# Performance work log

Hardware: AMD Instinct MI355X
Metric: run time of the kernel (lower is better)

## Reference

```python
import jax, jax.numpy as jnp
import numpy as np

N, D, E, R, G, M = 8192, 1024, 64, 64, 8, 8

def setup_inputs() -> dict:
    key = jax.random.key(0)
    k_h, k_wg, k_wl, k_w1, k_w2 = jax.random.split(key, 5)
    return {
        'h': jax.random.normal(k_h, (N, D), jnp.float32),
        'Wg': jax.random.normal(k_wg, (D, G), jnp.float32) * 0.02,  # nn.Linear weight (transposed)
        'bg': jnp.zeros((G,), jnp.float32),
        'Wloc': jax.random.normal(k_wl, (G, D, M), jnp.float32) * 0.02,
        'W1': jax.random.normal(k_w1, (E, D, R), jnp.float32) * 0.02,
        'W2': jax.random.normal(k_w2, (E, R, D), jnp.float32) * 0.02,
        'k': 2,
    }

def reference(h, Wg, bg, Wloc, W1, W2, k):
    n, d = h.shape
    g, _, m = Wloc.shape
    e = W1.shape[0]
    router_temp = 1.0
    # stage 1: group routing (top-1)
    g_scores = h @ Wg + bg                                   # (N, G)
    group_idx = jnp.argmax(g_scores, axis=-1)                # (N,)
    # stage 2: within-group scores; compute all groups (cheap: N*G*M) then select
    all_local = jnp.einsum('nd,gdm->ngm', h, Wloc)           # (N, G, M)
    local_scores = jnp.take_along_axis(all_local, group_idx[:, None, None], axis=1)[:, 0]  # (N, M)
    topv, topm = jax.lax.top_k(local_scores, k)              # (N, k)
    gate = jax.nn.softmax(topv / max(router_temp, 1e-6), axis=-1)
    expert_ids = group_idx[:, None] * m + topm               # (N, k) global expert ids
    # scatter gates into dense (N, E); topm entries are distinct per token
    gate_full = jnp.zeros((n, e), h.dtype).at[jnp.arange(n)[:, None], expert_ids].set(gate)
    # low-rank expert compute: relu(h @ W1) @ W2, weighted-combined
    tmp = jax.nn.relu(jnp.einsum('nd,edr->ner', h, W1))      # (N, E, R)
    out = jnp.einsum('ner,erd->nd', gate_full[:, :, None] * tmp, W2)  # (N, D)
    return out, expert_ids, gate, group_idx
```

## Files before the change

kernel.cpp:

```cpp
#include <hip/hip_runtime.h>
#include <hip/hip_bf16.h>
#include <cstdint>
#include <cstddef>

#define NTOK 8192
#define DIM  1024
#define NEXP 64
#define RANK 64
#define NGRP 8
#define NLOC 8

typedef __attribute__((ext_vector_type(8))) short bf16x8;
typedef __attribute__((ext_vector_type(4))) float f32x4;

static __device__ inline unsigned int pack_bf16x2(float a, float b) {
    __hip_bfloat16 ha = __float2bfloat16(a);
    __hip_bfloat16 hb = __float2bfloat16(b);
    return (unsigned int)(*(unsigned short*)&ha) |
           ((unsigned int)(*(unsigned short*)&hb) << 16);
}

__global__ __launch_bounds__(256, 4) void score_fused(
    const float* __restrict__ h, const float* __restrict__ Wg,
    const float* __restrict__ bg, const float* __restrict__ Wloc,
    unsigned short* __restrict__ hb, float* __restrict__ out_gidx,
    float* __restrict__ out_eid, float* __restrict__ out_gate,
    int* __restrict__ ws_eids, float* __restrict__ ws_gates,
    int* __restrict__ counts_e)
{
    __shared__ float Hs[16][66];
    __shared__ float Bs[64 * 8];
    __shared__ float Sp[16][16][8];
    __shared__ float Sg[16][9];
    __shared__ int   gsel[16];

    const int t0  = blockIdx.x * 16;
    const int tid = threadIdx.x;
    const int t   = tid & 15;
    const int kq  = tid >> 4;
    const int kbase = (kq >> 2) * 16 + (kq & 3);

    float acc[8] = {};
    for (int kc = 0; kc < DIM; kc += 64) {
        __syncthreads();
        {
            const int r = tid >> 4, c4 = tid & 15;
            const float4 v = *(const float4*)(h + (size_t)(t0 + r) * DIM + kc + c4 * 4);
            *(float2*)&Hs[r][c4 * 4]     = make_float2(v.x, v.y);
            *(float2*)&Hs[r][c4 * 4 + 2] = make_float2(v.z, v.w);
            uint2 pk;
            pk.x = pack_bf16x2(v.x, v.y);
            pk.y = pack_bf16x2(v.z, v.w);
            *(uint2*)(hb + (size_t)(t0 + r) * DIM + kc + c4 * 4) = pk;
        }
        {
            const float* src = Wg + (size_t)kc * NGRP;
            Bs[tid] = src[tid];
            Bs[tid + 256] = src[tid + 256];
        }
        __syncthreads();
#pragma unroll
        for (int kk = 0; kk < 4; ++kk) {
            const int k = kbase + kk * 4;
            const float a = Hs[t][k];
            const float4 b0 = *(const float4*)&Bs[k * 8];
            const float4 b1 = *(const float4*)&Bs[k * 8 + 4];
            acc[0] += a * b0.x; acc[1] += a * b0.y; acc[2] += a * b0.z; acc[3] += a * b0.w;
            acc[4] += a * b1.x; acc[5] += a * b1.y; acc[6] += a * b1.z; acc[7] += a * b1.w;
        }
    }
#pragma unroll
    for (int m = 0; m < 8; ++m) Sp[t][kq][m] = acc[m];
    __syncthreads();
    if (tid < 128) {
        const int tt = tid >> 3, m = tid & 7;
        float s = 0.f;
#pragma unroll
        for (int q = 0; q < 16; ++q) s += Sp[tt][q][m];
        Sg[tt][m] = s + bg[m];
    }
    __syncthreads();
    if (tid < 16) {
        int gi = 0; float best = Sg[tid][0];
#pragma unroll
        for (int g = 1; g < NGRP; ++g) {
            if (Sg[tid][g] > best) { best = Sg[tid][g]; gi = g; }
        }
        out_gidx[t0 + tid] = (float)gi;
        gsel[tid] = gi;
    }
    __syncthreads();

    {
        const int gsel_t = gsel[t];
        const float* wl = Wloc + (size_t)gsel_t * DIM * NLOC;
        const float* hrow = h + (size_t)(t0 + t) * DIM;
        float acc2[8] = {};
        for (int kc = DIM - 64; kc >= 0; kc -= 64) {
            const int k0 = kc + kq * 4;
            const f32x4 hv = *(const f32x4*)(hrow + k0);
#pragma unroll
            for (int kk = 0; kk < 4; ++kk) {
                const float a = hv[kk];
                const float4 b0 = *(const float4*)(wl + (size_t)(k0 + kk) * NLOC);
                const float4 b1 = *(const float4*)(wl + (size_t)(k0 + kk) * NLOC + 4);
                acc2[0] += a * b0.x; acc2[1] += a * b0.y; acc2[2] += a * b0.z; acc2[3] += a * b0.w;
                acc2[4] += a * b1.x; acc2[5] += a * b1.y; acc2[6] += a * b1.z; acc2[7] += a * b1.w;
            }
        }
#pragma unroll
        for (int m = 0; m < 8; ++m) Sp[t][kq][m] = acc2[m];
    }
    __syncthreads();
    if (tid < 128) {
        const int tt = tid >> 3, m = tid & 7;
        float s = 0.f;
#pragma unroll
        for (int q = 0; q < 16; ++q) s += Sp[tt][q][m];
        Sg[tt][m] = s;
    }
    __syncthreads();

    if (tid < 16) {
        const int tok = t0 + tid;
        float ls[NLOC];
#pragma unroll
        for (int m = 0; m < NLOC; ++m) ls[m] = Sg[tid][m];

        int m1 = 0; float v1 = ls[0];
#pragma unroll
        for (int m = 1; m < NLOC; ++m) { if (ls[m] > v1) { v1 = ls[m]; m1 = m; } }
        int m2 = (m1 == 0) ? 1 : 0; float v2 = ls[m2];
#pragma unroll
        for (int m = 0; m < NLOC; ++m) {
            if (m != m1 && m != ((m1 == 0) ? 1 : 0) && ls[m] > v2) { v2 = ls[m]; m2 = m; }
        }
        const float e2v = expf(v2 - v1);
        const float inv = 1.f / (1.f + e2v);
        const float g0 = inv, g1 = e2v * inv;
        const int gi = gsel[tid];
        const int ea = gi * NLOC + m1, eb = gi * NLOC + m2;

        out_eid[tok * 2 + 0] = (float)ea;
        out_eid[tok * 2 + 1] = (float)eb;
        out_gate[tok * 2 + 0] = g0;
        out_gate[tok * 2 + 1] = g1;
        ws_eids[tok * 2 + 0] = ea;
        ws_eids[tok * 2 + 1] = eb;
        ws_gates[tok * 2 + 0] = g0;
        ws_gates[tok * 2 + 1] = g1;
        atomicAdd(&counts_e[ea], 1);
        atomicAdd(&counts_e[eb], 1);
    }
}

__global__ __launch_bounds__(256) void scatter_e(
    const int* __restrict__ ws_eids, const float* __restrict__ ws_gates,
    const int* __restrict__ counts_e, int* __restrict__ cursor,
    int* __restrict__ token_list, float* __restrict__ slot_gate)
{
    __shared__ int offS[64];
    const int tid = threadIdx.x;
    if (tid < 64) {
        const int c = counts_e[tid];
        int s = c;
#pragma unroll
        for (int d = 1; d < 64; d <<= 1) {
            int v = __shfl_up(s, d, 64);
            if (tid >= d) s += v;
        }
        offS[tid] = s - c;
    }
    __syncthreads();
    const int t = blockIdx.x * 256 + tid;
    if (t >= NTOK) return;
#pragma unroll
    for (int j = 0; j < 2; ++j) {
        const int eid = ws_eids[t * 2 + j];
        const int pos = offS[eid] + atomicAdd(&cursor[eid], 1);
        token_list[pos] = t * 2 + j;
        slot_gate[pos] = ws_gates[t * 2 + j];
    }
}

__global__ __launch_bounds__(256) void prep_w(
    const float* __restrict__ W1, const float* __restrict__ W2,
    unsigned short* __restrict__ W1t, unsigned short* __restrict__ W2t)
{
    __shared__ float Ls[64][65];
    const int e = blockIdx.x;
    const int y = blockIdx.y;
    if (y < 16) {
        const int kb = y;
        const float* src = W1 + (size_t)e * DIM * RANK + (size_t)kb * 64 * RANK;
#pragma unroll
        for (int it = 0; it < 4; ++it) {
            const int kk = (threadIdx.x >> 4) + it * 16;
            const int rr = (threadIdx.x & 15) * 4;
            *(float4*)&Ls[kk][rr] = *(const float4*)(src + (size_t)kk * RANK + rr);
        }
        __syncthreads();
#pragma unroll
        for (int it = 0; it < 2; ++it) {
            const int idx = threadIdx.x + it * 256;
            const int r = idx >> 3, k8 = (idx & 7) * 8;
            uint4 v;
            v.x = pack_bf16x2(Ls[k8 + 0][r], Ls[k8 + 1][r]);
            v.y = pack_bf16x2(Ls[k8 + 2][r], Ls[k8 + 3][r]);
            v.z = pack_bf16x2(Ls[k8 + 4][r], Ls[k8 + 5][r]);
            v.w = pack_bf16x2(Ls[k8 + 6][r], Ls[k8 + 7][r]);
            *(uint4*)(W1t + (size_t)e * RANK * DIM + (size_t)r * DIM + kb * 64 + k8) = v;
        }
    } else {
        const int db = y - 16;
        const float* src = W2 + (size_t)e * RANK * DIM + db * 64;
#pragma unroll
        for (int it = 0; it < 4; ++it) {
            const int rr = (threadIdx.x >> 4) + it * 16;
            const int dd = (threadIdx.x & 15) * 4;
            *(float4*)&Ls[rr][dd] = *(const float4*)(src + (size_t)rr * DIM + dd);
        }
        __syncthreads();
#pragma unroll
        for (int it = 0; it < 2; ++it) {
            const int idx = threadIdx.x + it * 256;
            const int d = idx >> 3, r8 = (idx & 7) * 8;
            uint4 v;
            v.x = pack_bf16x2(Ls[r8 + 0][d], Ls[r8 + 1][d]);
            v.y = pack_bf16x2(Ls[r8 + 2][d], Ls[r8 + 3][d]);
            v.z = pack_bf16x2(Ls[r8 + 4][d], Ls[r8 + 5][d]);
            v.w = pack_bf16x2(Ls[r8 + 6][d], Ls[r8 + 7][d]);
            *(uint4*)(W2t + (size_t)e * DIM * RANK + (size_t)(db * 64 + d) * RANK + r8) = v;
        }
    }
}

__global__ __launch_bounds__(256, 2) void e1_mfma(
    const unsigned short* __restrict__ hb, const unsigned short* __restrict__ W1t,
    const int* __restrict__ counts_e, const int* __restrict__ token_list,
    const float* __restrict__ slot_gate, unsigned short* __restrict__ P)
{
    __shared__ unsigned short Hs[64 * 72];
    __shared__ unsigned short Ws[64 * 72];
    __shared__ int   tokS[64];
    __shared__ float gateS[64];
    __shared__ int   offS[65];

    const int e   = blockIdx.x;
    const int tid = threadIdx.x;
    if (tid < 64) {
        const int c = counts_e[tid];
        int s = c;
#pragma unroll
        for (int d = 1; d < 64; d <<= 1) {
            int v = __shfl_up(s, d, 64);
            if (tid >= d) s += v;
        }
        offS[tid] = s - c;
        if (tid == 63) offS[64] = s;
    }
    __syncthreads();
    const int n0 = offS[e];
    const int ne = offS[e + 1] - n0;

    const unsigned short* W1te = W1t + (size_t)e * RANK * DIM;
    const int wave = tid >> 6;
    const int lane = tid & 63;
    const int tx   = lane & 15;
    const int quad = lane >> 4;

    for (int tile = blockIdx.y; tile * 64 < ne; tile += 8) {
        const int row0 = tile * 64;
        __syncthreads();
        if (tid < 64) {
            const int gr = row0 + tid;
            tokS[tid]  = (gr < ne) ? token_list[n0 + gr] : -1;
            gateS[tid] = (gr < ne) ? slot_gate[n0 + gr] : 0.f;
        }
        f32x4 acc[4] = {};
        for (int kc = 0; kc < DIM; kc += 64) {
            __syncthreads();
#pragma unroll
            for (int it = 0; it < 2; ++it) {
                const int idx = tid + it * 256;
                const int s = idx >> 3, k8 = (idx & 7) * 8;
                const int ent = tokS[s];
                uint4 v = make_uint4(0, 0, 0, 0);
                if (ent >= 0)
                    v = *(const uint4*)(hb + (size_t)(ent >> 1) * DIM + kc + k8);
                *(uint4*)(Hs + s * 72 + k8) = v;
            }
#pragma unroll
            for (int it = 0; it < 2; ++it) {
                const int idx = tid + it * 256;
                const int r = idx >> 3, k8 = (idx & 7) * 8;
                *(uint4*)(Ws + r * 72 + k8) =
                    *(const uint4*)(W1te + (size_t)r * DIM + kc + k8);
            }
            __syncthreads();
#pragma unroll
            for (int ks = 0; ks < 2; ++ks) {
                const bf16x8 a = *(const bf16x8*)(Hs + (wave * 16 + tx) * 72 + ks * 32 + quad * 8);
#pragma unroll
                for (int j = 0; j < 4; ++j) {
                    const bf16x8 b = *(const bf16x8*)(Ws + (j * 16 + tx) * 72 + ks * 32 + quad * 8);
                    acc[j] = __builtin_amdgcn_mfma_f32_16x16x32_bf16(a, b, acc[j], 0, 0, 0);
                }
            }
        }
#pragma unroll
        for (int j = 0; j < 4; ++j) {
#pragma unroll
            for (int i = 0; i < 4; ++i) {
                const int sl = wave * 16 + quad * 4 + i;
                const int gr = row0 + sl;
                if (gr < ne) {
                    const float v = fmaxf(acc[j][i], 0.f) * gateS[sl];
                    __hip_bfloat16 hv = __float2bfloat16(v);
                    P[(size_t)(n0 + gr) * RANK + j * 16 + tx] = *(unsigned short*)&hv;
                }
            }
        }
    }
}

__global__ __launch_bounds__(256, 2) void e2_mfma(
    const unsigned short* __restrict__ P, const unsigned short* __restrict__ W2t,
    const int* __restrict__ counts_e, const int* __restrict__ token_list,
    float* __restrict__ out, float* __restrict__ contrib)
{
    __shared__ unsigned short Ps[64 * 72];
    __shared__ unsigned short W2s[64 * 72];
    __shared__ int tokS[64];
    __shared__ int offS[65];

    const int e = blockIdx.x;
    const int colbase = blockIdx.y * 64;
    const int tid = threadIdx.x;
    if (tid < 64) {
        const int c = counts_e[tid];
        int s = c;
#pragma unroll
        for (int d = 1; d < 64; d <<= 1) {
            int v = __shfl_up(s, d, 64);
            if (tid >= d) s += v;
        }
        offS[tid] = s - c;
        if (tid == 63) offS[64] = s;
    }
    __syncthreads();
    const int n0 = offS[e];
    const int ne = offS[e + 1] - n0;

    const unsigned short* W2te = W2t + (size_t)e * DIM * RANK;
    const int wave = tid >> 6;
    const int lane = tid & 63;
    const int tx   = lane & 15;
    const int quad = lane >> 4;

#pragma unroll
    for (int it = 0; it < 2; ++it) {
        const int idx = tid + it * 256;
        const int d = idx >> 3, r8 = (idx & 7) * 8;
        *(uint4*)(W2s + d * 72 + r8) =
            *(const uint4*)(W2te + (size_t)(colbase + d) * RANK + r8);
    }

    for (int tile = blockIdx.z; tile * 64 < ne; tile += 4) {
        const int row0 = tile * 64;
        __syncthreads();
        if (tid < 64) {
            const int gr = row0 + tid;
            tokS[tid] = (gr < ne) ? token_list[n0 + gr] : -1;
        }
#pragma unroll
        for (int it = 0; it < 2; ++it) {
            const int idx = tid + it * 256;
            const int s = idx >> 3, r8 = (idx & 7) * 8;
            const int gr = row0 + s;
            uint4 v = make_uint4(0, 0, 0, 0);
            if (gr < ne) v = *(const uint4*)(P + (size_t)(n0 + gr) * RANK + r8);
            *(uint4*)(Ps + s * 72 + r8) = v;
        }
        __syncthreads();
        f32x4 acc[4] = {};
#pragma unroll
        for (int ks = 0; ks < 2; ++ks) {
            const bf16x8 a = *(const bf16x8*)(Ps + (wave * 16 + tx) * 72 + ks * 32 + quad * 8);
#pragma unroll
            for (int j = 0; j < 4; ++j) {
                const bf16x8 b = *(const bf16x8*)(W2s + (j * 16 + tx) * 72 + ks * 32 + quad * 8);
                acc[j] = __builtin_amdgcn_mfma_f32_16x16x32_bf16(a, b, acc[j], 0, 0, 0);
            }
        }
#pragma unroll
        for (int i = 0; i < 4; ++i) {
            const int sl = wave * 16 + quad * 4 + i;
            const int ent = tokS[sl];
            if (ent >= 0) {
                float* base = (ent & 1) ? contrib : out;
                float* op = base + (size_t)(ent >> 1) * DIM + colbase;
#pragma unroll
                for (int j = 0; j < 4; ++j)
                    op[j * 16 + tx] = acc[j][i];
            }
        }
    }
}

__global__ __launch_bounds__(256) void combine_kernel(
    const float* __restrict__ contrib, float* __restrict__ out)
{
    const size_t i = (size_t)blockIdx.x * 256 + threadIdx.x;
    float4 a = ((const float4*)out)[i];
    const float4 b = ((const float4*)contrib)[i];
    a.x += b.x; a.y += b.y; a.z += b.z; a.w += b.w;
    ((float4*)out)[i] = a;
}

extern "C" void kernel_launch(void* const* d_in, const int* in_sizes, int n_in,
                              void* d_out, int out_size, void* d_ws, size_t ws_size,
                              hipStream_t stream)
{
    const float* h    = (const float*)d_in[0];
    const float* Wg   = (const float*)d_in[1];
    const float* bg   = (const float*)d_in[2];
    const float* Wloc = (const float*)d_in[3];
    const float* W1   = (const float*)d_in[4];
    const float* W2   = (const float*)d_in[5];

    float* out_f    = (float*)d_out;
    float* out_main = out_f;
    float* out_eid  = out_f + (size_t)NTOK * DIM;
    float* out_gate = out_eid + (size_t)NTOK * 2;
    float* out_gidx = out_gate + (size_t)NTOK * 2;

    int* ws_i        = (int*)d_ws;
    int* counts_e    = ws_i;
    int* cursor_e    = ws_i + 192;
    int* ws_eids     = ws_i + 16896;
    int* token_list  = ws_i + 33280;
    float* ws_f      = (float*)(ws_i + 49664);
    float* ws_gates  = ws_f;
    float* slot_gate = ws_f + 16384;
    unsigned short* P_h = (unsigned short*)(ws_f + 2 * 16384 + 65536);
    unsigned short* W1t = P_h + (size_t)16384 * RANK;
    unsigned short* W2t = W1t + (size_t)NEXP * RANK * DIM;
    float* contrib      = (float*)(W2t + (size_t)NEXP * DIM * RANK);
    unsigned short* hb = (unsigned short*)contrib;

    hipMemsetAsync(ws_i, 0, 256 * sizeof(int), stream);

    prep_w<<<dim3(NEXP, 32), 256, 0, stream>>>(W1, W2, W1t, W2t);
    score_fused<<<NTOK / 16, 256, 0, stream>>>(h, Wg, bg, Wloc, hb,
        out_gidx, out_eid, out_gate, ws_eids, ws_gates, counts_e);
    scatter_e<<<NTOK / 256, 256, 0, stream>>>(ws_eids, ws_gates, counts_e,
        cursor_e, token_list, slot_gate);
    e1_mfma<<<dim3(NEXP, 8), 256, 0, stream>>>(hb, W1t, counts_e, token_list,
        slot_gate, P_h);
    e2_mfma<<<dim3(NEXP, 16, 4), 256, 0, stream>>>(P_h, W2t, counts_e, token_list,
        out_main, contrib);
    combine_kernel<<<(NTOK * DIM / 4) / 256, 256, 0, stream>>>(contrib, out_main);
}
```

Baseline: 263.7 us.

## Restructure routing kernel to one wavefront per token with shuffle reductions

```diff
diff --git a/kernel.cpp b/kernel.cpp
--- a/kernel.cpp
+++ b/kernel.cpp
@@ -20,7 +20,7 @@
            ((unsigned int)(*(unsigned short*)&hb) << 16);
 }
 
-__global__ __launch_bounds__(256, 4) void score_fused(
+__global__ __launch_bounds__(256, 8) void score_route(
     const float* __restrict__ h, const float* __restrict__ Wg,
     const float* __restrict__ bg, const float* __restrict__ Wloc,
     unsigned short* __restrict__ hb, float* __restrict__ out_gidx,
@@ -28,119 +28,101 @@
     int* __restrict__ ws_eids, float* __restrict__ ws_gates,
     int* __restrict__ counts_e)
 {
-    __shared__ float Hs[16][66];
-    __shared__ float Bs[64 * 8];
-    __shared__ float Sp[16][16][8];
-    __shared__ float Sg[16][9];
-    __shared__ int   gsel[16];
-
-    const int t0  = blockIdx.x * 16;
-    const int tid = threadIdx.x;
-    const int t   = tid & 15;
-    const int kq  = tid >> 4;
-    const int kbase = (kq >> 2) * 16 + (kq & 3);
-
-    float acc[8] = {};
-    for (int kc = 0; kc < DIM; kc += 64) {
-        __syncthreads();
-        {
-            const int r = tid >> 4, c4 = tid & 15;
-            const float4 v = *(const float4*)(h + (size_t)(t0 + r) * DIM + kc + c4 * 4);
-            *(float2*)&Hs[r][c4 * 4]     = make_float2(v.x, v.y);
-            *(float2*)&Hs[r][c4 * 4 + 2] = make_float2(v.z, v.w);
-            uint2 pk;
-            pk.x = pack_bf16x2(v.x, v.y);
-            pk.y = pack_bf16x2(v.z, v.w);
-            *(uint2*)(hb + (size_t)(t0 + r) * DIM + kc + c4 * 4) = pk;
-        }
-        {
-            const float* src = Wg + (size_t)kc * NGRP;
-            Bs[tid] = src[tid];
-            Bs[tid + 256] = src[tid + 256];
-        }
-        __syncthreads();
-#pragma unroll
-        for (int kk = 0; kk < 4; ++kk) {
-            const int k = kbase + kk * 4;
-            const float a = Hs[t][k];
-            const float4 b0 = *(const float4*)&Bs[k * 8];
-            const float4 b1 = *(const float4*)&Bs[k * 8 + 4];
-            acc[0] += a * b0.x; acc[1] += a * b0.y; acc[2] += a * b0.z; acc[3] += a * b0.w;
-            acc[4] += a * b1.x; acc[5] += a * b1.y; acc[6] += a * b1.z; acc[7] += a * b1.w;
-        }
-    }
-#pragma unroll
-    for (int m = 0; m < 8; ++m) Sp[t][kq][m] = acc[m];
-    __syncthreads();
-    if (tid < 128) {
-        const int tt = tid >> 3, m = tid & 7;
-        float s = 0.f;
-#pragma unroll
-        for (int q = 0; q < 16; ++q) s += Sp[tt][q][m];
-        Sg[tt][m] = s + bg[m];
-    }
-    __syncthreads();
-    if (tid < 16) {
-        int gi = 0; float best = Sg[tid][0];
-#pragma unroll
-        for (int g = 1; g < NGRP; ++g) {
-            if (Sg[tid][g] > best) { best = Sg[tid][g]; gi = g; }
-        }
-        out_gidx[t0 + tid] = (float)gi;
-        gsel[tid] = gi;
-    }
-    __syncthreads();
-
-    {
-        const int gsel_t = gsel[t];
-        const float* wl = Wloc + (size_t)gsel_t * DIM * NLOC;
-        const float* hrow = h + (size_t)(t0 + t) * DIM;
-        float acc2[8] = {};
-        for (int kc = DIM - 64; kc >= 0; kc -= 64) {
-            const int k0 = kc + kq * 4;
-            const f32x4 hv = *(const f32x4*)(hrow + k0);
-#pragma unroll
-            for (int kk = 0; kk < 4; ++kk) {
-                const float a = hv[kk];
-                const float4 b0 = *(const float4*)(wl + (size_t)(k0 + kk) * NLOC);
-                const float4 b1 = *(const float4*)(wl + (size_t)(k0 + kk) * NLOC + 4);
-                acc2[0] += a * b0.x; acc2[1] += a * b0.y; acc2[2] += a * b0.z; acc2[3] += a * b0.w;
-                acc2[4] += a * b1.x; acc2[5] += a * b1.y; acc2[6] += a * b1.z; acc2[7] += a * b1.w;
-            }
-        }
-#pragma unroll
-        for (int m = 0; m < 8; ++m) Sp[t][kq][m] = acc2[m];
-    }
-    __syncthreads();
-    if (tid < 128) {
-        const int tt = tid >> 3, m = tid & 7;
-        float s = 0.f;
-#pragma unroll
-        for (int q = 0; q < 16; ++q) s += Sp[tt][q][m];
-        Sg[tt][m] = s;
-    }
-    __syncthreads();
-
-    if (tid < 16) {
-        const int tok = t0 + tid;
-        float ls[NLOC];
-#pragma unroll
-        for (int m = 0; m < NLOC; ++m) ls[m] = Sg[tid][m];
-
-        int m1 = 0; float v1 = ls[0];
-#pragma unroll
-        for (int m = 1; m < NLOC; ++m) { if (ls[m] > v1) { v1 = ls[m]; m1 = m; } }
-        int m2 = (m1 == 0) ? 1 : 0; float v2 = ls[m2];
-#pragma unroll
-        for (int m = 0; m < NLOC; ++m) {
-            if (m != m1 && m != ((m1 == 0) ? 1 : 0) && ls[m] > v2) { v2 = ls[m]; m2 = m; }
-        }
+    __shared__ float hLds[4][1024];
+
+    const int tid  = threadIdx.x;
+    const int wave = tid >> 6;
+    const int lane = tid & 63;
+    const int tok  = blockIdx.x * 4 + wave;
+
+    const float* hrow = h + (size_t)tok * DIM;
+    unsigned short* hbrow = hb + (size_t)tok * DIM;
+
+    float4 hv[4];
+#pragma unroll
+    for (int i = 0; i < 4; ++i)
+        hv[i] = *(const float4*)(hrow + lane * 4 + i * 256);
+#pragma unroll
+    for (int i = 0; i < 4; ++i) {
+        const int k0 = lane * 4 + i * 256;
+        *(float4*)&hLds[wave][k0] = hv[i];
+        uint2 pk;
+        pk.x = pack_bf16x2(hv[i].x, hv[i].y);
+        pk.y = pack_bf16x2(hv[i].z, hv[i].w);
+        *(uint2*)(hbrow + k0) = pk;
+    }
+
+    const int row_l = lane >> 1;
+    const int half  = lane & 1;
+
+    float ga[4] = {};
+#pragma unroll 8
+    for (int i = 0; i < 32; ++i) {
+        const float a  = hLds[wave][i * 32 + row_l];
+        const float4 b = *(const float4*)(Wg + i * 256 + lane * 4);
+        ga[0] += a * b.x; ga[1] += a * b.y; ga[2] += a * b.z; ga[3] += a * b.w;
+    }
+#pragma unroll
+    for (int d = 2; d < 64; d <<= 1) {
+#pragma unroll
+        for (int m = 0; m < 4; ++m) ga[m] += __shfl_xor(ga[m], d, 64);
+    }
+    float gb[4];
+#pragma unroll
+    for (int m = 0; m < 4; ++m) gb[m] = __shfl_xor(ga[m], 1, 64);
+
+    float sc[8];
+#pragma unroll
+    for (int m = 0; m < 4; ++m) {
+        sc[m]     = (half ? gb[m] : ga[m]) + bg[m];
+        sc[m + 4] = (half ? ga[m] : gb[m]) + bg[m + 4];
+    }
+    int gi = 0; float best = sc[0];
+#pragma unroll
+    for (int g = 1; g < NGRP; ++g) {
+        if (sc[g] > best) { best = sc[g]; gi = g; }
+    }
+
+    const float* wl = Wloc + (size_t)gi * (DIM * NLOC);
+    float la[4] = {};
+#pragma unroll 8
+    for (int i = 0; i < 32; ++i) {
+        const float a  = hLds[wave][i * 32 + row_l];
+        const float4 b = *(const float4*)(wl + i * 256 + lane * 4);
+        la[0] += a * b.x; la[1] += a * b.y; la[2] += a * b.z; la[3] += a * b.w;
+    }
+#pragma unroll
+    for (int d = 2; d < 64; d <<= 1) {
+#pragma unroll
+        for (int m = 0; m < 4; ++m) la[m] += __shfl_xor(la[m], d, 64);
+    }
+    float lb[4];
+#pragma unroll
+    for (int m = 0; m < 4; ++m) lb[m] = __shfl_xor(la[m], 1, 64);
+
+    float ls[8];
+#pragma unroll
+    for (int m = 0; m < 4; ++m) {
+        ls[m]     = half ? lb[m] : la[m];
+        ls[m + 4] = half ? la[m] : lb[m];
+    }
+
+    int m1 = 0; float v1 = ls[0];
+#pragma unroll
+    for (int m = 1; m < NLOC; ++m) { if (ls[m] > v1) { v1 = ls[m]; m1 = m; } }
+    int m2 = (m1 == 0) ? 1 : 0; float v2 = ls[m2];
+#pragma unroll
+    for (int m = 0; m < NLOC; ++m) {
+        if (m != m1 && m != ((m1 == 0) ? 1 : 0) && ls[m] > v2) { v2 = ls[m]; m2 = m; }
+    }
+
+    if (lane == 0) {
         const float e2v = expf(v2 - v1);
         const float inv = 1.f / (1.f + e2v);
         const float g0 = inv, g1 = e2v * inv;
-        const int gi = gsel[tid];
         const int ea = gi * NLOC + m1, eb = gi * NLOC + m2;
 
+        out_gidx[tok] = (float)gi;
         out_eid[tok * 2 + 0] = (float)ea;
         out_eid[tok * 2 + 1] = (float)eb;
         out_gate[tok * 2 + 0] = g0;
@@ -452,7 +434,7 @@
     hipMemsetAsync(ws_i, 0, 256 * sizeof(int), stream);
 
     prep_w<<<dim3(NEXP, 32), 256, 0, stream>>>(W1, W2, W1t, W2t);
-    score_fused<<<NTOK / 16, 256, 0, stream>>>(h, Wg, bg, Wloc, hb,
+    score_route<<<NTOK / 4, 256, 0, stream>>>(h, Wg, bg, Wloc, hb,
         out_gidx, out_eid, out_gate, ws_eids, ws_gates, counts_e);
     scatter_e<<<NTOK / 256, 256, 0, stream>>>(ws_eids, ws_gates, counts_e,
         cursor_e, token_list, slot_gate);
```

After: 289.9 us. +9.9%, slower.
